# Kernel optimization log

Measured on AMD Instinct MI355X. Metric: run time of the kernel, lower is better.

## Reference

```python
import jax, jax.numpy as jnp
import numpy as np

N = 10000  # number of graph nodes
K = 16     # number of clusters


def setup_inputs() -> dict:
    key = jax.random.key(0)
    k1, k2, k3 = jax.random.split(key, 3)
    adj = jax.random.uniform(k1, (N, N), dtype=jnp.float32)
    att = jax.random.uniform(k2, (N, N), dtype=jnp.float32)
    output = jax.random.uniform(k3, (N, K), dtype=jnp.float32)
    return {"adj": adj, "att": att, "output": output}


def reference(adj, att, output):
    # Faithful to SubClusteringLoss.forward. The original computes
    # diag(output @ (A @ output).T), which is mathematically identical to the
    # row-wise dot sum(output * (A @ output), axis=1); we use the O(N*K) form
    # instead of materializing the wasted [N, N] product.
    sub_num_edges = jnp.sum(adj)

    adj_multi_out = adj @ output                                  # [N, K]
    sub_structure_loss = jnp.sum(output * adj_multi_out, axis=1) / sub_num_edges  # [N]

    att_multi_out = att @ output                                  # [N, K]
    sub_attribute_loss = jnp.sum(output * att_multi_out, axis=1) / sub_num_edges  # [N]

    cluster_size = jnp.sum(output, axis=0)                        # [K]
    n_nodes = output.shape[0]
    n_clusters = output.shape[1]
    regularization_loss = (
        jnp.linalg.norm(cluster_size) / n_nodes * jnp.sqrt(jnp.float32(n_clusters)) - 1.0
    )

    clu_loss = -(jnp.sum(sub_structure_loss) + jnp.sum(sub_attribute_loss) - regularization_loss)
    return (
        clu_loss,
        -sub_structure_loss,
        -sub_attribute_loss,
        -(sub_structure_loss + sub_attribute_loss),
    )
```

## Files before the change

### kernel.cpp

```cpp
#include <hip/hip_runtime.h>
#include <math.h>

namespace {

constexpr int N = 10000;
constexpr int K = 16;
constexpr int JT = 1024;
constexpr int ROWS_PER_BLOCK = 32;
constexpr int TILES = (N + ROWS_PER_BLOCK - 1) / ROWS_PER_BLOCK;


__global__ __launch_bounds__(512, 4)
void scl_main(const float* __restrict__ adj, const float* __restrict__ att,
              const float* __restrict__ outm, float* __restrict__ ws,
              float* __restrict__ d_out) {
  __shared__ float planes[K][JT];

  const int bx = blockIdx.x;
  const int m = (bx >= TILES) ? 1 : 0;
  const int tile = bx - m * TILES;
  const float* __restrict__ A = m ? att : adj;
  const int wave = threadIdx.x >> 6;
  const int lane = threadIdx.x & 63;
  const int r0 = tile * ROWS_PER_BLOCK + wave * 4;
  const bool wv = (r0 + 4) <= N;

  float acc0[K], acc1[K], acc2[K], acc3[K];
#pragma unroll
  for (int k = 0; k < K; ++k) { acc0[k] = 0.f; acc1[k] = 0.f; acc2[k] = 0.f; acc3[k] = 0.f; }
  float rsum = 0.f;
  const float* Ar = A + (size_t)r0 * N;

  for (int c = 0; c < (N + JT - 1) / JT; ++c) {
    const int jbase = c * JT;
    const int clen = (N - jbase) < JT ? (N - jbase) : JT;

    for (int idx = threadIdx.x; idx < (clen << 2); idx += 512) {
      const int jj = idx >> 2;
      const int q = idx & 3;
      const float4 v = *(const float4*)(outm + ((size_t)(jbase + jj) << 4) + (q << 2));
      planes[q * 4 + 0][jj] = v.x;
      planes[q * 4 + 1][jj] = v.y;
      planes[q * 4 + 2][jj] = v.z;
      planes[q * 4 + 3][jj] = v.w;
    }
    __syncthreads();

    if (wv) {
      for (int it = 0; it < 4; ++it) {
        const int jl = (it << 8) + (lane << 2);
        if (jl < clen) {
          const float* p = Ar + jbase + jl;
          const float4 a0 = *(const float4*)(p);
          const float4 a1 = *(const float4*)(p + N);
          const float4 a2 = *(const float4*)(p + 2 * N);
          const float4 a3 = *(const float4*)(p + 3 * N);
          rsum += (a0.x + a0.y + a0.z + a0.w) + (a1.x + a1.y + a1.z + a1.w) +
                  (a2.x + a2.y + a2.z + a2.w) + (a3.x + a3.y + a3.z + a3.w);
#pragma unroll
          for (int k = 0; k < K; ++k) {
            const float4 o = *(const float4*)&planes[k][jl];
            acc0[k] += a0.x * o.x + a0.y * o.y + a0.z * o.z + a0.w * o.w;
            acc1[k] += a1.x * o.x + a1.y * o.y + a1.z * o.z + a1.w * o.w;
            acc2[k] += a2.x * o.x + a2.y * o.y + a2.z * o.z + a2.w * o.w;
            acc3[k] += a3.x * o.x + a3.y * o.y + a3.z * o.z + a3.w * o.w;
          }
        }
      }
    }
    __syncthreads();
  }

  float p0 = 0.f, p1 = 0.f, p2 = 0.f, p3 = 0.f;
  if (wv) {
    const float* o0 = outm + (size_t)r0 * K;
#pragma unroll
    for (int k = 0; k < K; ++k) {
      p0 += o0[k] * acc0[k];
      p1 += o0[K + k] * acc1[k];
      p2 += o0[2 * K + k] * acc2[k];
      p3 += o0[3 * K + k] * acc3[k];
    }
  }
#pragma unroll
  for (int off = 32; off >= 1; off >>= 1) {
    p0 += __shfl_xor(p0, off, 64);
    p1 += __shfl_xor(p1, off, 64);
    p2 += __shfl_xor(p2, off, 64);
    p3 += __shfl_xor(p3, off, 64);
    rsum += __shfl_xor(rsum, off, 64);
  }
  if (lane == 0 && wv) {
    float* dst = d_out + 1 + m * N + r0;
    dst[0] = p0; dst[1] = p1; dst[2] = p2; dst[3] = p3;
    atomicAdd(&ws[1 + m], p0 + p1 + p2 + p3);
    if (m == 0) atomicAdd(&ws[0], rsum);
  }
}

__global__ void scl_colsum(const float* __restrict__ outm, float* __restrict__ ws) {
  __shared__ float red[16][17];
  const int k = threadIdx.x & 15;
  const int g = threadIdx.x >> 4;
  float acc = 0.f;
  for (int r = blockIdx.x * 16 + g; r < N; r += gridDim.x * 16)
    acc += outm[(size_t)r * K + k];
  red[g][k] = acc;
  __syncthreads();
  if (threadIdx.x < 16) {
    float s = 0.f;
#pragma unroll
    for (int gg = 0; gg < 16; ++gg) s += red[gg][threadIdx.x];
    atomicAdd(&ws[4 + threadIdx.x], s);
  }
}

__global__ void scl_finalize(float* __restrict__ d_out, const float* __restrict__ ws) {
  const float S = ws[0];
  const float inv = 1.0f / S;
  const int i = blockIdx.x * blockDim.x + threadIdx.x;
  if (i < N) {
    const float su = d_out[1 + i];
    const float au = d_out[1 + N + i];
    d_out[1 + i] = -su * inv;
    d_out[1 + N + i] = -au * inv;
    d_out[1 + 2 * N + i] = -(su + au) * inv;
  }
  if (blockIdx.x == 0 && threadIdx.x == 0) {
    float cs2 = 0.f;
#pragma unroll
    for (int k = 0; k < K; ++k) cs2 += ws[4 + k] * ws[4 + k];
    const float reg = sqrtf(cs2) / (float)N * 4.0f - 1.0f;
    d_out[0] = -((ws[1] + ws[2]) * inv - reg);
  }
}

}

extern "C" void kernel_launch(void* const* d_in, const int* in_sizes, int n_in,
                              void* d_out, int out_size, void* d_ws, size_t ws_size,
                              hipStream_t stream) {
  const float* adj  = (const float*)d_in[0];
  const float* att  = (const float*)d_in[1];
  const float* outm = (const float*)d_in[2];
  float* out = (float*)d_out;
  float* ws = (float*)d_ws;

  hipMemsetAsync(d_ws, 0, 32 * sizeof(float), stream);
  scl_colsum<<<32, 256, 0, stream>>>(outm, ws);
  scl_main<<<2 * TILES, 512, 0, stream>>>(adj, att, outm, ws, out);
  scl_finalize<<<(N + 255) / 256, 256, 0, stream>>>(out, ws);
}
```

Baseline: 934.8 us.

## Split column range across blocks and shrink tiles for higher occupancy

Partitions each row's column range into four independent chunks handled by separate blocks, with fewer rows per wave and smaller tiles, and combines partial row dots with atomics into a zeroed output. Edge sum is accumulated in double via one atomic per block, and the final scalar loss is reduced in a single-block finalize. This aims to raise occupancy and memory-level parallelism on a bandwidth-bound matvec. In exchange it adds more shared-memory reloads of the output matrix per byte of A, many more atomics, and an extra memset.

```diff
diff --git a/kernel.cpp b/kernel.cpp
--- a/kernel.cpp
+++ b/kernel.cpp
@@ -5,40 +5,48 @@
 
 constexpr int N = 10000;
 constexpr int K = 16;
-constexpr int JT = 1024;
-constexpr int ROWS_PER_BLOCK = 32;
-constexpr int TILES = (N + ROWS_PER_BLOCK - 1) / ROWS_PER_BLOCK;
+constexpr int JT = 256;
+constexpr int RPB = 8;
+constexpr int TILES = N / RPB;
+constexpr int JU = 4;
+constexpr int JX = N / JU;
+constexpr int NCH = (JX + JT - 1) / JT;
 
 
-__global__ __launch_bounds__(512, 4)
+__global__ __launch_bounds__(256, 6)
 void scl_main(const float* __restrict__ adj, const float* __restrict__ att,
               const float* __restrict__ outm, float* __restrict__ ws,
               float* __restrict__ d_out) {
   __shared__ float planes[K][JT];
+  __shared__ float rred[4];
 
   const int bx = blockIdx.x;
-  const int m = (bx >= TILES) ? 1 : 0;
-  const int tile = bx - m * TILES;
+  const int m = (bx >= TILES * JU) ? 1 : 0;
+  const int t = bx - m * TILES * JU;
+  const int ju = t / TILES;
+  const int tile = t - ju * TILES;
   const float* __restrict__ A = m ? att : adj;
   const int wave = threadIdx.x >> 6;
   const int lane = threadIdx.x & 63;
-  const int r0 = tile * ROWS_PER_BLOCK + wave * 4;
-  const bool wv = (r0 + 4) <= N;
+  const int r0 = tile * RPB + wave * 2;
+  const int j0 = ju * JX;
 
-  float acc0[K], acc1[K], acc2[K], acc3[K];
+  float acc0[K], acc1[K];
 #pragma unroll
-  for (int k = 0; k < K; ++k) { acc0[k] = 0.f; acc1[k] = 0.f; acc2[k] = 0.f; acc3[k] = 0.f; }
+  for (int k = 0; k < K; ++k) { acc0[k] = 0.f; acc1[k] = 0.f; }
   float rsum = 0.f;
-  const float* Ar = A + (size_t)r0 * N;
+  const float* __restrict__ Ar = A + (size_t)r0 * N + j0;
 
-  for (int c = 0; c < (N + JT - 1) / JT; ++c) {
-    const int jbase = c * JT;
-    const int clen = (N - jbase) < JT ? (N - jbase) : JT;
+#pragma unroll 1
+  for (int c = 0; c < NCH; ++c) {
+    const int jb = j0 + c * JT;
+    const int rem = JX - c * JT;
+    const int clen = rem < JT ? rem : JT;
 
-    for (int idx = threadIdx.x; idx < (clen << 2); idx += 512) {
+    for (int idx = threadIdx.x; idx < (clen << 2); idx += 256) {
       const int jj = idx >> 2;
       const int q = idx & 3;
-      const float4 v = *(const float4*)(outm + ((size_t)(jbase + jj) << 4) + (q << 2));
+      const float4 v = *(const float4*)(outm + ((size_t)(jb + jj) << 4) + (q << 2));
       planes[q * 4 + 0][jj] = v.x;
       planes[q * 4 + 1][jj] = v.y;
       planes[q * 4 + 2][jj] = v.z;
@@ -46,55 +54,46 @@
     }
     __syncthreads();
 
-    if (wv) {
-      for (int it = 0; it < 4; ++it) {
-        const int jl = (it << 8) + (lane << 2);
-        if (jl < clen) {
-          const float* p = Ar + jbase + jl;
-          const float4 a0 = *(const float4*)(p);
-          const float4 a1 = *(const float4*)(p + N);
-          const float4 a2 = *(const float4*)(p + 2 * N);
-          const float4 a3 = *(const float4*)(p + 3 * N);
-          rsum += (a0.x + a0.y + a0.z + a0.w) + (a1.x + a1.y + a1.z + a1.w) +
-                  (a2.x + a2.y + a2.z + a2.w) + (a3.x + a3.y + a3.z + a3.w);
+    const int jl = lane << 2;
+    if (jl < clen) {
+      const float* p = Ar + c * JT + jl;
+      const float4 a0 = *(const float4*)(p);
+      const float4 a1 = *(const float4*)(p + N);
+      if (m == 0)
+        rsum += (a0.x + a0.y + a0.z + a0.w) + (a1.x + a1.y + a1.z + a1.w);
 #pragma unroll
-          for (int k = 0; k < K; ++k) {
-            const float4 o = *(const float4*)&planes[k][jl];
-            acc0[k] += a0.x * o.x + a0.y * o.y + a0.z * o.z + a0.w * o.w;
-            acc1[k] += a1.x * o.x + a1.y * o.y + a1.z * o.z + a1.w * o.w;
-            acc2[k] += a2.x * o.x + a2.y * o.y + a2.z * o.z + a2.w * o.w;
-            acc3[k] += a3.x * o.x + a3.y * o.y + a3.z * o.z + a3.w * o.w;
-          }
-        }
+      for (int k = 0; k < K; ++k) {
+        const float4 o = *(const float4*)&planes[k][jl];
+        acc0[k] += a0.x * o.x + a0.y * o.y + a0.z * o.z + a0.w * o.w;
+        acc1[k] += a1.x * o.x + a1.y * o.y + a1.z * o.z + a1.w * o.w;
       }
     }
     __syncthreads();
   }
 
-  float p0 = 0.f, p1 = 0.f, p2 = 0.f, p3 = 0.f;
-  if (wv) {
-    const float* o0 = outm + (size_t)r0 * K;
+  float p0 = 0.f, p1 = 0.f;
+  const float* o0 = outm + (size_t)r0 * K;
 #pragma unroll
-    for (int k = 0; k < K; ++k) {
-      p0 += o0[k] * acc0[k];
-      p1 += o0[K + k] * acc1[k];
-      p2 += o0[2 * K + k] * acc2[k];
-      p3 += o0[3 * K + k] * acc3[k];
-    }
+  for (int k = 0; k < K; ++k) {
+    p0 += o0[k] * acc0[k];
+    p1 += o0[K + k] * acc1[k];
   }
 #pragma unroll
   for (int off = 32; off >= 1; off >>= 1) {
     p0 += __shfl_xor(p0, off, 64);
     p1 += __shfl_xor(p1, off, 64);
-    p2 += __shfl_xor(p2, off, 64);
-    p3 += __shfl_xor(p3, off, 64);
     rsum += __shfl_xor(rsum, off, 64);
   }
-  if (lane == 0 && wv) {
-    float* dst = d_out + 1 + m * N + r0;
-    dst[0] = p0; dst[1] = p1; dst[2] = p2; dst[3] = p3;
-    atomicAdd(&ws[1 + m], p0 + p1 + p2 + p3);
-    if (m == 0) atomicAdd(&ws[0], rsum);
+  if (lane == 0) {
+    atomicAdd(&d_out[1 + m * N + r0], p0);
+    atomicAdd(&d_out[1 + m * N + r0 + 1], p1);
+    rred[wave] = rsum;
+  }
+  __syncthreads();
+  if (threadIdx.x == 0 && m == 0) {
+    const double rb = (double)rred[0] + (double)rred[1] +
+                      (double)rred[2] + (double)rred[3];
+    atomicAdd((double*)ws, rb);
   }
 }
 
@@ -116,22 +115,33 @@
 }
 
 __global__ void scl_finalize(float* __restrict__ d_out, const float* __restrict__ ws) {
-  const float S = ws[0];
-  const float inv = 1.0f / S;
-  const int i = blockIdx.x * blockDim.x + threadIdx.x;
-  if (i < N) {
+  __shared__ float red[1024];
+  const double S = *(const double*)ws;
+  const float inv = (float)(1.0 / S);
+
+  float tsum = 0.f;
+  for (int i = threadIdx.x; i < 2 * N; i += 1024) tsum += d_out[1 + i];
+  red[threadIdx.x] = tsum;
+  __syncthreads();
+#pragma unroll
+  for (int s = 512; s > 0; s >>= 1) {
+    if (threadIdx.x < s) red[threadIdx.x] += red[threadIdx.x + s];
+    __syncthreads();
+  }
+
+  for (int i = threadIdx.x; i < N; i += 1024) {
     const float su = d_out[1 + i];
     const float au = d_out[1 + N + i];
     d_out[1 + i] = -su * inv;
     d_out[1 + N + i] = -au * inv;
     d_out[1 + 2 * N + i] = -(su + au) * inv;
   }
-  if (blockIdx.x == 0 && threadIdx.x == 0) {
+  if (threadIdx.x == 0) {
     float cs2 = 0.f;
 #pragma unroll
     for (int k = 0; k < K; ++k) cs2 += ws[4 + k] * ws[4 + k];
     const float reg = sqrtf(cs2) / (float)N * 4.0f - 1.0f;
-    d_out[0] = -((ws[1] + ws[2]) * inv - reg);
+    d_out[0] = -(red[0] * inv - reg);
   }
 }
 
@@ -147,7 +157,8 @@
   float* ws = (float*)d_ws;
 
   hipMemsetAsync(d_ws, 0, 32 * sizeof(float), stream);
+  hipMemsetAsync((char*)d_out + sizeof(float), 0, 2 * N * sizeof(float), stream);
   scl_colsum<<<32, 256, 0, stream>>>(outm, ws);
-  scl_main<<<2 * TILES, 512, 0, stream>>>(adj, att, outm, ws, out);
-  scl_finalize<<<(N + 255) / 256, 256, 0, stream>>>(out, ws);
+  scl_main<<<2 * TILES * JU, 256, 0, stream>>>(adj, att, outm, ws, out);
+  scl_finalize<<<1, 1024, 0, stream>>>(out, ws);
 }
```

Result: faster. 853.1 us (-8.7%).
